# Performance work log

Hardware: AMD Instinct MI355X
Metric: run time of the kernel (lower is better)

The kernel has to match this reference:

```python
import jax, jax.numpy as jnp
import numpy as np

NEG_SLOPE = 0.2
EPS = 1e-5

N_NODES = 50000
N_GRAPHS = 500
NODES_PER_GRAPH = 100
N_EDGES = 500000
F_IN = 16
F_GRAPH = 4
HID = 64
N_CLASSES = 2


def setup_inputs() -> dict:
    key = jax.random.key(0)
    ks = jax.random.split(key, 32)
    x = jax.random.normal(ks[0], (N_NODES, F_IN), dtype=jnp.float32)
    # intra-graph random edges: dst lives in the same 100-node block as src
    src = jax.random.randint(ks[1], (N_EDGES,), 0, N_NODES)
    dst = (src // NODES_PER_GRAPH) * NODES_PER_GRAPH + jax.random.randint(ks[2], (N_EDGES,), 0, NODES_PER_GRAPH)
    edge_index = jnp.stack([src, dst]).astype(jnp.int64)
    graph_input = jax.random.normal(ks[3], (N_GRAPHS, F_GRAPH), dtype=jnp.float32)
    batch = (jnp.arange(N_NODES) // NODES_PER_GRAPH).astype(jnp.int64)

    def w(k, shape, scale=0.1):
        return (jax.random.normal(k, shape, dtype=jnp.float32) * scale)

    inp = dict(x=x, edge_index=edge_index, graph_input=graph_input, batch=batch)
    # GraphNorm params
    inp['gn_w'] = jnp.ones((F_IN,), jnp.float32)
    inp['gn_b'] = w(ks[4], (F_IN,))
    inp['gn_ms'] = jnp.ones((F_IN,), jnp.float32)
    inp['W1'] = w(ks[5], (F_IN, 4 * HID))
    inp['as1'] = w(ks[6], (4, HID)); inp['ad1'] = w(ks[7], (4, HID))
    inp['b1'] = w(ks[8], (4 * HID,))
    inp['W2'] = w(ks[9], (4 * HID, 4 * HID))
    inp['as2'] = w(ks[10], (4, HID)); inp['ad2'] = w(ks[11], (4, HID))
    inp['b2'] = w(ks[12], (4 * HID,))
    inp['W3'] = w(ks[13], (4 * HID, HID))
    inp['as3'] = w(ks[14], (1, HID)); inp['ad3'] = w(ks[15], (1, HID))
    inp['b3'] = w(ks[16], (HID,))
    # BatchNorm1d (eval mode) over [HID + F_GRAPH]
    D = HID + F_GRAPH
    inp['bn_g'] = 1.0 + w(ks[17], (D,))
    inp['bn_b'] = w(ks[18], (D,))
    inp['bn_m'] = jnp.zeros((D,), jnp.float32)
    inp['bn_v'] = jnp.ones((D,), jnp.float32)
    # Dense head
    inp['Wd1'] = w(ks[19], (D, HID)); inp['bd1'] = w(ks[20], (HID,))
    inp['Wd2'] = w(ks[21], (HID, HID)); inp['bd2'] = w(ks[22], (HID,))
    inp['Wo'] = w(ks[23], (HID, N_CLASSES)); inp['bo'] = w(ks[24], (N_CLASSES,))
    return inp


def _segment_softmax(e, seg, n):
    m = jax.ops.segment_max(e, seg, num_segments=n)
    ex = jnp.exp(e - m[seg])
    s = jax.ops.segment_sum(ex, seg, num_segments=n)
    return ex / s[seg]


def _gat_conv(x, src, dst, W, att_src, att_dst, b):
    N = x.shape[0]
    H, C = att_src.shape
    loop = jnp.arange(N)
    src = jnp.concatenate([src, loop])  # PyG GATConv adds self-loops
    dst = jnp.concatenate([dst, loop])
    h = (x @ W).reshape(N, H, C)
    a_src = (h * att_src).sum(-1)  # [N,H]
    a_dst = (h * att_dst).sum(-1)
    e = jax.nn.leaky_relu(a_src[src] + a_dst[dst], NEG_SLOPE)  # [E,H]
    alpha = _segment_softmax(e, dst, N)
    out = jax.ops.segment_sum(h[src] * alpha[:, :, None], dst, num_segments=N)
    return out.reshape(N, H * C) + b


def _graph_norm(x, batch, n_graphs, w, b, ms):
    cnt = jax.ops.segment_sum(jnp.ones((x.shape[0],), x.dtype), batch, num_segments=n_graphs)[:, None]
    mean = jax.ops.segment_sum(x, batch, num_segments=n_graphs) / cnt
    out = x - mean[batch] * ms
    var = jax.ops.segment_sum(out * out, batch, num_segments=n_graphs) / cnt
    return w * out / jnp.sqrt(var[batch] + EPS) + b


def _global_mean_pool(x, batch, n_graphs):
    cnt = jax.ops.segment_sum(jnp.ones((x.shape[0],), x.dtype), batch, num_segments=n_graphs)[:, None]
    return jax.ops.segment_sum(x, batch, num_segments=n_graphs) / cnt


def reference(x, edge_index, graph_input, batch,
              gn_w, gn_b, gn_ms,
              W1, as1, ad1, b1,
              W2, as2, ad2, b2,
              W3, as3, ad3, b3,
              bn_g, bn_b, bn_m, bn_v,
              Wd1, bd1, Wd2, bd2, Wo, bo):
    src, dst = edge_index[0], edge_index[1]
    G = graph_input.shape[0]
    h = _graph_norm(x, batch, G, gn_w, gn_b, gn_ms)
    # dropout is a no-op in eval
    h = jax.nn.elu(_gat_conv(h, src, dst, W1, as1, ad1, b1))
    h = jax.nn.elu(_gat_conv(h, src, dst, W2, as2, ad2, b2))
    h = _gat_conv(h, src, dst, W3, as3, ad3, b3)
    g = _global_mean_pool(h, batch, G)
    g = jnp.concatenate([g, graph_input], axis=1)
    g = (g - bn_m) / jnp.sqrt(bn_v + EPS) * bn_g + bn_b  # BatchNorm1d eval
    g = jax.nn.selu(g @ Wd1 + bd1)
    g = jax.nn.selu(g @ Wd2 + bd2)
    g = g @ Wo + bo
    return jax.nn.softmax(g, axis=1)
```

## Files before the change

### kernel.cpp

```cpp
#include <hip/hip_runtime.h>
#include <math.h>

#define N_NODES 50000
#define N_ROWS_PAD 50048
#define N_GRAPHS 500
#define NPG 100
#define N_EDGES 500000
#define F_IN 16
#define HID 64
#define EW_CAP 1408

#define SELU_SCALE 1.0507009873554804934193349852946f
#define SELU_ALPHA 1.6732632423543772848170429916717f

typedef __attribute__((ext_vector_type(8))) short short8;
typedef __attribute__((ext_vector_type(8))) unsigned short ushort8;
typedef __attribute__((ext_vector_type(4))) float floatx4;

__device__ __forceinline__ float lrelu(float x){ return x > 0.f ? x : 0.2f * x; }
__device__ __forceinline__ float eluf(float x){ return x > 0.f ? x : expf(x) - 1.f; }
__device__ __forceinline__ float seluf(float x){
    return x > 0.f ? SELU_SCALE * x : SELU_SCALE * (SELU_ALPHA * (expf(x) - 1.f));
}
__device__ __forceinline__ unsigned short f2bf(float x){
    unsigned u = __float_as_uint(x);
    return (unsigned short)((u + 0x7FFFu + ((u >> 16) & 1u)) >> 16);
}
__device__ __forceinline__ float bf2f(unsigned short u){
    return __uint_as_float((unsigned)u << 16);
}
__device__ __forceinline__ float bf2f_lo(unsigned u){
    return __uint_as_float(u << 16);
}
__device__ __forceinline__ float bf2f_hi(unsigned u){
    return __uint_as_float(u & 0xFFFF0000u);
}

__global__ void k_count(const int* __restrict__ dst, int* __restrict__ counts){
    int e = blockIdx.x * 256 + threadIdx.x;
    if (e < N_EDGES) atomicAdd(&counts[dst[e]], 1);
}

__global__ void __launch_bounds__(128)
k_local_scan(const int* __restrict__ counts, int* __restrict__ noff,
             int* __restrict__ cnt, int* __restrict__ write_ptr){
    __shared__ int s[128];
    int g = blockIdx.x, t = threadIdx.x;
    int v = (t < NPG) ? counts[g * NPG + t] : 0;
    s[t] = v; __syncthreads();
    for (int o = 1; o < 128; o <<= 1){
        int x = (t >= o) ? s[t - o] : 0;
        __syncthreads();
        s[t] += x;
        __syncthreads();
    }
    if (t < NPG){
        int excl = s[t] - v;
        noff[g * NPG + t] = excl;
        cnt[g * NPG + t] = v;
        write_ptr[g * NPG + t] = excl;
    }
}

__global__ void k_scatter(const int* __restrict__ src, const int* __restrict__ dst,
                          int* __restrict__ write_ptr, unsigned* __restrict__ csr){
    int e = blockIdx.x * 256 + threadIdx.x;
    if (e < N_EDGES){
        int d = dst[e];
        int g = d / NPG;
        int b = g * NPG;
        int pos = atomicAdd(&write_ptr[d], 1);
        csr[(size_t)g * EW_CAP + pos] = (unsigned)((src[e] - b) | ((d - b) << 8));
    }
}

__global__ void k_prep(const float* __restrict__ W1, const float* __restrict__ as1,
                       const float* __restrict__ ad1,
                       const float* __restrict__ W2, const float* __restrict__ as2,
                       const float* __restrict__ ad2,
                       const float* __restrict__ W3, const float* __restrict__ as3,
                       const float* __restrict__ ad3,
                       unsigned short* __restrict__ Wp2, unsigned short* __restrict__ Wp3,
                       float* __restrict__ M1f,
                       unsigned short* __restrict__ Mp2, unsigned short* __restrict__ Mp3){
    int id = blockIdx.x * 256 + threadIdx.x;
    if (id < 65536){
        int k = id >> 8, o = id & 255;
        int srccol = (o & 3) * 64 + (o >> 2);
        Wp2[(((k >> 3) * 256) + o) * 8 + (k & 7)] = f2bf(W2[k * 256 + srccol]);
    } else if (id < 81920){
        int i = id - 65536;
        int k = i >> 6, n = i & 63;
        Wp3[(((k >> 3) * 64) + n) * 8 + (k & 7)] = f2bf(W3[i]);
    } else if (id < 82048){
        int i = id - 81920;
        int k = i >> 3, j = i & 7;
        int h = j & 3;
        const float* a = (j < 4) ? as1 : ad1;
        float s = 0.f;
        for (int c = 0; c < 64; c++) s += W1[k * 256 + h * 64 + c] * a[h * 64 + c];
        M1f[k * 8 + j] = s;
    } else if (id < 86144){
        int i = id - 82048;
        int k = i >> 4, col = i & 15;
        float s = 0.f;
        if (col < 8){
            int h = col & 3;
            const float* a = (col < 4) ? as2 : ad2;
            for (int c = 0; c < 64; c++) s += W2[k * 256 + h * 64 + c] * a[h * 64 + c];
        }
        Mp2[((k >> 3) * 16 + col) * 8 + (k & 7)] = f2bf(s);
    } else if (id < 90240){
        int i = id - 86144;
        int k = i >> 4, col = i & 15;
        float s = 0.f;
        if (col < 2){
            const float* a = (col == 0) ? as3 : ad3;
            for (int c = 0; c < 64; c++) s += W3[k * 64 + c] * a[c];
        }
        Mp3[((k >> 3) * 16 + col) * 8 + (k & 7)] = f2bf(s);
    }
}

__global__ void __launch_bounds__(256)
k_gnorm_conv1(const float* __restrict__ x, const float* __restrict__ w,
              const float* __restrict__ b, const float* __restrict__ ms,
              const float* __restrict__ W1, const float* __restrict__ M1f,
              unsigned short* __restrict__ Ybf, float* __restrict__ lg1){
    __shared__ float sx[NPG * F_IN];
    __shared__ float Ws[16][256];
    __shared__ float red[16][16];
    __shared__ float meanS[16], varS[16];
    int g = blockIdx.x, t = threadIdx.x;
    int base = g * NPG;
    for (int idx = t; idx < NPG * F_IN; idx += 256) sx[idx] = x[base * F_IN + idx];
    for (int i = t; i < 1024; i += 256)
        *(float4*)&Ws[0][i * 4] = *(const float4*)&W1[i * 4];
    __syncthreads();
    int f = t & 15, grp = t >> 4;
    float p = 0.f;
    for (int i = grp; i < NPG; i += 16) p += sx[i * 16 + f];
    red[grp][f] = p; __syncthreads();
    if (t < 16){
        float s = 0.f;
        for (int i = 0; i < 16; i++) s += red[i][t];
        meanS[t] = s * (1.f / 100.f);
    }
    __syncthreads();
    float mm = meanS[f] * ms[f];
    p = 0.f;
    for (int i = grp; i < NPG; i += 16){ float v = sx[i * 16 + f] - mm; p += v * v; }
    red[grp][f] = p; __syncthreads();
    if (t < 16){
        float s = 0.f;
        for (int i = 0; i < 16; i++) s += red[i][t];
        varS[t] = s * (1.f / 100.f);
    }
    __syncthreads();
    for (int idx = t; idx < NPG * F_IN; idx += 256){
        int ff = idx & 15;
        sx[idx] = w[ff] * (sx[idx] - meanS[ff] * ms[ff]) * rsqrtf(varS[ff] + 1e-5f) + b[ff];
    }
    __syncthreads();
    int c4 = t & 15, rsub = t >> 4;
    for (int n = rsub; n < NPG; n += 16){
        float acc[16];
        #pragma unroll
        for (int j = 0; j < 16; j++) acc[j] = 0.f;
        #pragma unroll
        for (int k = 0; k < 16; k++){
            float a_ = sx[n * 16 + k];
            float4 b0 = *(const float4*)&Ws[k][c4 * 4];
            float4 b1 = *(const float4*)&Ws[k][64 + c4 * 4];
            float4 b2 = *(const float4*)&Ws[k][128 + c4 * 4];
            float4 b3 = *(const float4*)&Ws[k][192 + c4 * 4];
            float bv[16] = {b0.x, b0.y, b0.z, b0.w, b1.x, b1.y, b1.z, b1.w,
                            b2.x, b2.y, b2.z, b2.w, b3.x, b3.y, b3.z, b3.w};
            #pragma unroll
            for (int j = 0; j < 16; j++) acc[j] = fmaf(a_, bv[j], acc[j]);
        }
        ushort8 ua, ub;
        #pragma unroll
        for (int m = 0; m < 8; m++){
            ua[m] = f2bf(acc[(m & 3) * 4 + (m >> 2)]);
            ub[m] = f2bf(acc[(m & 3) * 4 + 2 + (m >> 2)]);
        }
        size_t ob = (size_t)(base + n) * 256 + c4 * 16;
        *(ushort8*)&Ybf[ob]     = ua;
        *(ushort8*)&Ybf[ob + 8] = ub;
    }
    for (int i = t; i < NPG * 8; i += 256){
        int n = i >> 3, j = i & 7;
        float s = 0.f;
        #pragma unroll
        for (int ff = 0; ff < 16; ff++) s += sx[n * 16 + ff] * M1f[ff * 8 + j];
        lg1[(size_t)(base + n) * 8 + j] = s;
    }
}

template<int COLB, int LG>
__global__ void __launch_bounds__(256)
k_gemm_mfma(const unsigned short* __restrict__ Xb,
            const unsigned short* __restrict__ Wp,
            const unsigned short* __restrict__ Mp,
            unsigned short* __restrict__ Ybf, float* __restrict__ lg,
            int N, int K, int OUT){
    int b = blockIdx.x;
    if (COLB == 4){
        int xcd = b & 7, idx = b >> 3;
        b = xcd * (int)(gridDim.x >> 3) + idx;
    }
    int cb = b & (COLB - 1);
    int rb = b / COLB;

    int t = threadIdx.x;
    int wave = t >> 6, lane = t & 63;
    int quad = lane >> 4, ln = lane & 15;
    int r0 = rb * 64 + wave * 16;
    int c0 = cb * 64;

    floatx4 acc[4];
    #pragma unroll
    for (int f = 0; f < 4; f++) acc[f] = (floatx4){0.f, 0.f, 0.f, 0.f};
    floatx4 accL = (floatx4){0.f, 0.f, 0.f, 0.f};

    const unsigned short* aptr = Xb + (size_t)(r0 + ln) * K + quad * 8;
    for (int kt = 0; kt < K; kt += 32){
        short8 a = *(const short8*)(aptr + kt);
        int kc = (kt >> 3) + quad;
        #pragma unroll
        for (int f = 0; f < 4; f++){
            short8 bfr = *(const short8*)(Wp + ((size_t)kc * OUT + c0 + f * 16 + ln) * 8);
            acc[f] = __builtin_amdgcn_mfma_f32_16x16x32_bf16(a, bfr, acc[f], 0, 0, 0);
        }
        if (LG > 0){
            if (cb == 0){
                short8 m = *(const short8*)(Mp + ((size_t)kc * 16 + ln) * 8);
                accL = __builtin_amdgcn_mfma_f32_16x16x32_bf16(a, m, accL, 0, 0, 0);
            }
        }
    }
    int rowb = r0 + quad * 4;
    #pragma unroll
    for (int f = 0; f < 4; f++){
        int col = c0 + f * 16 + ln;
        #pragma unroll
        for (int rg = 0; rg < 4; rg++){
            int row = rowb + rg;
            if (row < N) Ybf[(size_t)row * OUT + col] = f2bf(acc[f][rg]);
        }
    }
    if (LG > 0){
        if (cb == 0 && ln < LG){
            #pragma unroll
            for (int rg = 0; rg < 4; rg++){
                int row = rowb + rg;
                if (row < N) lg[(size_t)row * LG + ln] = accL[rg];
            }
        }
    }
}

__global__ void __launch_bounds__(512)
k_fused4(const unsigned short* __restrict__ hbf, const float* __restrict__ lg,
         const float* __restrict__ bias,
         const unsigned* __restrict__ csr, const int* __restrict__ noff,
         const int* __restrict__ cnt, unsigned short* __restrict__ out_bf){
    __shared__ __align__(16) unsigned int edl[EW_CAP][4];
    __shared__ __align__(16) float asrcl[NPG * 4], adstl[NPG * 4];
    __shared__ __align__(16) float wselfl[NPG * 4], rsuml[NPG * 4];
    __shared__ int offl[NPG], cntl[NPG];

    int g = blockIdx.x, t = threadIdx.x;
    int wave = t >> 6, lane = t & 63;
    int base = g * NPG;
    size_t ebeg = (size_t)g * EW_CAP;

    if (t < NPG){
        offl[t] = noff[base + t];
        cntl[t] = cnt[base + t];
        const float* lp = lg + (size_t)(base + t) * 8;
        *(float4*)&asrcl[t * 4] = *(const float4*)lp;
        *(float4*)&adstl[t * 4] = *(const float4*)(lp + 4);
    }
    __syncthreads();
    int eln = offl[NPG - 1] + cntl[NPG - 1];
    for (int i = t; i < eln; i += 512) edl[i][2] = csr[ebeg + i];
    __syncthreads();

    for (int i = t; i < eln; i += 512){
        unsigned sd = edl[i][2];
        int s = sd & 0xFF, d = sd >> 8;
        float4 av = *(const float4*)&asrcl[s * 4];
        float4 dv = *(const float4*)&adstl[d * 4];
        unsigned w0 = f2bf(expf(lrelu(av.x + dv.x)));
        unsigned w1 = f2bf(expf(lrelu(av.y + dv.y)));
        unsigned w2 = f2bf(expf(lrelu(av.z + dv.z)));
        unsigned w3 = f2bf(expf(lrelu(av.w + dv.w)));
        edl[i][0] = w0 | (w1 << 16);
        edl[i][1] = w2 | (w3 << 16);
    }
    __syncthreads();

    if (t < NPG){
        int d = t;
        float4 av = *(const float4*)&asrcl[d * 4];
        float4 dv = *(const float4*)&adstl[d * 4];
        float ws0 = expf(lrelu(av.x + dv.x));
        float ws1 = expf(lrelu(av.y + dv.y));
        float ws2 = expf(lrelu(av.z + dv.z));
        float ws3 = expf(lrelu(av.w + dv.w));
        float s0 = ws0, s1 = ws1, s2 = ws2, s3 = ws3;
        int ebg = offl[d], n = cntl[d];
        for (int j = 0; j < n; j++){
            uint2 v = *(const uint2*)&edl[ebg + j][0];
            s0 += bf2f_lo(v.x); s1 += bf2f_hi(v.x);
            s2 += bf2f_lo(v.y); s3 += bf2f_hi(v.y);
        }
        *(float4*)&wselfl[d * 4] = make_float4(ws0, ws1, ws2, ws3);
        *(float4*)&rsuml[d * 4]  = make_float4(1.f / s0, 1.f / s1, 1.f / s2, 1.f / s3);
    }
    __syncthreads();

    float b0 = bias[lane], b1 = bias[64 + lane], b2 = bias[128 + lane], b3 = bias[192 + lane];
    for (int d = wave; d < NPG; d += 8){
        float4 ws = *(const float4*)&wselfl[d * 4];
        float4 rs = *(const float4*)&rsuml[d * 4];
        ushort4 hv = *(const ushort4*)&hbf[(size_t)(base + d) * 256 + lane * 4];
        float a0 = ws.x * bf2f(hv.x);
        float a1 = ws.y * bf2f(hv.y);
        float a2 = ws.z * bf2f(hv.z);
        float a3 = ws.w * bf2f(hv.w);
        int ebg = offl[d], n = cntl[d];
        int j = 0;
        #pragma unroll 1
        for (; j + 4 <= n; j += 4){
            #pragma unroll
            for (int k = 0; k < 4; k++){
                uint4 v = *(const uint4*)&edl[ebg + j + k][0];
                int s = (int)(v.z & 0xFFu);
                ushort4 x = *(const ushort4*)&hbf[(size_t)(base + s) * 256 + lane * 4];
                a0 = fmaf(bf2f_lo(v.x), bf2f(x.x), a0);
                a1 = fmaf(bf2f_hi(v.x), bf2f(x.y), a1);
                a2 = fmaf(bf2f_lo(v.y), bf2f(x.z), a2);
                a3 = fmaf(bf2f_hi(v.y), bf2f(x.w), a3);
            }
        }
        for (; j < n; j++){
            uint4 v = *(const uint4*)&edl[ebg + j][0];
            int s = (int)(v.z & 0xFFu);
            ushort4 x = *(const ushort4*)&hbf[(size_t)(base + s) * 256 + lane * 4];
            a0 = fmaf(bf2f_lo(v.x), bf2f(x.x), a0);
            a1 = fmaf(bf2f_hi(v.x), bf2f(x.y), a1);
            a2 = fmaf(bf2f_lo(v.y), bf2f(x.z), a2);
            a3 = fmaf(bf2f_hi(v.y), bf2f(x.w), a3);
        }
        size_t ob = (size_t)(base + d) * 256 + lane;
        out_bf[ob]       = f2bf(eluf(a0 * rs.x + b0));
        out_bf[ob + 64]  = f2bf(eluf(a1 * rs.y + b1));
        out_bf[ob + 128] = f2bf(eluf(a2 * rs.z + b2));
        out_bf[ob + 192] = f2bf(eluf(a3 * rs.w + b3));
    }
}

__global__ void __launch_bounds__(512)
k_fused1(const unsigned short* __restrict__ hbf, const float* __restrict__ lg3,
         const float* __restrict__ bias,
         const unsigned* __restrict__ csr, const int* __restrict__ noff,
         const int* __restrict__ cnt, float* __restrict__ out){
    __shared__ __align__(16) unsigned int edl[EW_CAP][2];
    __shared__ float asrcl[NPG], adstl[NPG];
    __shared__ float wselfl[NPG], rsuml[NPG];
    __shared__ int offl[NPG], cntl[NPG];

    int g = blockIdx.x, t = threadIdx.x;
    int wave = t >> 6, lane = t & 63;
    int base = g * NPG;
    size_t ebeg = (size_t)g * EW_CAP;

    if (t < NPG){
        offl[t] = noff[base + t];
        cntl[t] = cnt[base + t];
        asrcl[t] = lg3[(size_t)(base + t) * 2];
        adstl[t] = lg3[(size_t)(base + t) * 2 + 1];
    }
    __syncthreads();
    int eln = offl[NPG - 1] + cntl[NPG - 1];
    for (int i = t; i < eln; i += 512) edl[i][1] = csr[ebeg + i];
    __syncthreads();

    for (int i = t; i < eln; i += 512){
        unsigned sd = edl[i][1];
        int s = sd & 0xFF, d = sd >> 8;
        edl[i][0] = (unsigned)f2bf(expf(lrelu(asrcl[s] + adstl[d])));
    }
    __syncthreads();

    if (t < NPG){
        float wsf = expf(lrelu(asrcl[t] + adstl[t]));
        float sum = wsf;
        int ebg = offl[t], n = cntl[t];
        for (int j = 0; j < n; j++) sum += bf2f((unsigned short)edl[ebg + j][0]);
        wselfl[t] = wsf;
        rsuml[t] = 1.f / sum;
    }
    __syncthreads();

    float bl = bias[lane];
    for (int d = wave; d < NPG; d += 8){
        float acc = wselfl[d] * bf2f(hbf[(size_t)(base + d) * 64 + lane]);
        int ebg = offl[d], n = cntl[d];
        for (int j = 0; j < n; j++){
            uint2 v = *(const uint2*)&edl[ebg + j][0];
            acc = fmaf(bf2f_lo(v.x),
                       bf2f(hbf[(size_t)(base + (int)(v.y & 0xFFu)) * 64 + lane]), acc);
        }
        out[(size_t)(base + d) * 64 + lane] = acc * rsuml[d] + bl;
    }
}

__global__ void k_head(const float* __restrict__ x3, const float* __restrict__ gin,
                       const float* __restrict__ bn_g, const float* __restrict__ bn_b,
                       const float* __restrict__ bn_m, const float* __restrict__ bn_v,
                       const float* __restrict__ Wd1, const float* __restrict__ bd1,
                       const float* __restrict__ Wd2, const float* __restrict__ bd2,
                       const float* __restrict__ Wo, const float* __restrict__ bo,
                       float* __restrict__ out){
    __shared__ float red[256];
    __shared__ float gv[68];
    __shared__ float g2[64];
    __shared__ float g3[64];
    int g = blockIdx.x, t = threadIdx.x;
    int c = t & 63, grp = t >> 6;
    float p = 0.f;
    for (int i = grp; i < NPG; i += 4) p += x3[(g * NPG + i) * 64 + c];
    red[t] = p; __syncthreads();
    if (t < 64){
        float s = red[t] + red[t + 64] + red[t + 128] + red[t + 192];
        float mean = s * (1.f / 100.f);
        gv[t] = (mean - bn_m[t]) * rsqrtf(bn_v[t] + 1e-5f) * bn_g[t] + bn_b[t];
    } else if (t < 68){
        int j = t - 64;
        float v = gin[g * 4 + j];
        gv[t] = (v - bn_m[t]) * rsqrtf(bn_v[t] + 1e-5f) * bn_g[t] + bn_b[t];
    }
    __syncthreads();
    if (t < 64){
        float s = bd1[t];
        for (int i = 0; i < 68; i++) s += gv[i] * Wd1[i * 64 + t];
        g2[t] = seluf(s);
    }
    __syncthreads();
    if (t < 64){
        float s = bd2[t];
        for (int i = 0; i < 64; i++) s += g2[i] * Wd2[i * 64 + t];
        g3[t] = seluf(s);
    }
    __syncthreads();
    if (t == 0){
        float l0 = bo[0], l1 = bo[1];
        for (int i = 0; i < 64; i++){ l0 += g3[i] * Wo[i * 2]; l1 += g3[i] * Wo[i * 2 + 1]; }
        float mx = fmaxf(l0, l1);
        float e0 = expf(l0 - mx), e1 = expf(l1 - mx);
        float inv = 1.f / (e0 + e1);
        out[g * 2] = e0 * inv;
        out[g * 2 + 1] = e1 * inv;
    }
}

extern "C" void kernel_launch(void* const* d_in, const int* in_sizes, int n_in,
                              void* d_out, int out_size, void* d_ws, size_t ws_size,
                              hipStream_t stream){
    const float* x   = (const float*)d_in[0];
    const int*   ei  = (const int*)d_in[1];
    const float* gin = (const float*)d_in[2];
    const float* gn_w = (const float*)d_in[4];
    const float* gn_b = (const float*)d_in[5];
    const float* gn_ms = (const float*)d_in[6];
    const float* W1 = (const float*)d_in[7];
    const float* as1 = (const float*)d_in[8];
    const float* ad1 = (const float*)d_in[9];
    const float* b1 = (const float*)d_in[10];
    const float* W2 = (const float*)d_in[11];
    const float* as2 = (const float*)d_in[12];
    const float* ad2 = (const float*)d_in[13];
    const float* b2 = (const float*)d_in[14];
    const float* W3 = (const float*)d_in[15];
    const float* as3 = (const float*)d_in[16];
    const float* ad3 = (const float*)d_in[17];
    const float* b3 = (const float*)d_in[18];
    const float* bn_g = (const float*)d_in[19];
    const float* bn_b = (const float*)d_in[20];
    const float* bn_m = (const float*)d_in[21];
    const float* bn_v = (const float*)d_in[22];
    const float* Wd1 = (const float*)d_in[23];
    const float* bd1 = (const float*)d_in[24];
    const float* Wd2 = (const float*)d_in[25];
    const float* bd2 = (const float*)d_in[26];
    const float* Wo = (const float*)d_in[27];
    const float* bo = (const float*)d_in[28];
    float* out = (float*)d_out;

    const int* src = ei;
    const int* dst = ei + N_EDGES;

    char* ws = (char*)d_ws;
    size_t off = 0;
    auto alloc = [&](size_t bytes) -> void* {
        void* p = ws + off;
        off = (off + bytes + 255) & ~(size_t)255;
        return p;
    };
    int* counts     = (int*)alloc((size_t)N_NODES * 4);
    int* write_ptr  = (int*)alloc((size_t)N_NODES * 4);
    unsigned* csr   = (unsigned*)alloc((size_t)N_GRAPHS * EW_CAP * 4);
    int* noff       = (int*)alloc((size_t)N_NODES * 4);
    int* cnt        = (int*)alloc((size_t)N_NODES * 4);
    unsigned short* wp2 = (unsigned short*)alloc((size_t)256 * 256 * 2);
    unsigned short* wp3 = (unsigned short*)alloc((size_t)256 * 64 * 2);
    float* M1f      = (float*)alloc((size_t)16 * 8 * 4);
    unsigned short* Mp2 = (unsigned short*)alloc((size_t)32 * 16 * 8 * 2);
    unsigned short* Mp3 = (unsigned short*)alloc((size_t)32 * 16 * 8 * 2);
    float* lg1      = (float*)alloc((size_t)N_NODES * 8 * 4);
    float* lg2      = (float*)alloc((size_t)N_ROWS_PAD * 8 * 4);
    float* lg3      = (float*)alloc((size_t)N_ROWS_PAD * 2 * 4);
    unsigned short* xbh = (unsigned short*)alloc((size_t)N_NODES * 256 * 2);
    unsigned short* xb  = (unsigned short*)alloc((size_t)N_ROWS_PAD * 256 * 2);
    unsigned short* x3b = (unsigned short*)alloc((size_t)N_NODES * HID * 2);
    float* bufD     = (float*)alloc((size_t)N_NODES * HID * 4);

    hipMemsetAsync(counts, 0, (size_t)N_NODES * 4, stream);
    k_count<<<(N_EDGES + 255) / 256, 256, 0, stream>>>(dst, counts);
    k_prep<<<(90240 + 255) / 256, 256, 0, stream>>>(W1, as1, ad1, W2, as2, ad2,
                                                    W3, as3, ad3, wp2, wp3, M1f, Mp2, Mp3);
    k_local_scan<<<N_GRAPHS, 128, 0, stream>>>(counts, noff, cnt, write_ptr);
    k_scatter<<<(N_EDGES + 255) / 256, 256, 0, stream>>>(src, dst, write_ptr, csr);

    k_gnorm_conv1<<<N_GRAPHS, 256, 0, stream>>>(x, gn_w, gn_b, gn_ms, W1, M1f, xbh, lg1);
    k_fused4<<<N_GRAPHS, 512, 0, stream>>>(xbh, lg1, b1, csr, noff, cnt, xb);

    k_gemm_mfma<4, 8><<<(N_ROWS_PAD / 64) * 4, 256, 0, stream>>>(xb, wp2, Mp2, xbh, lg2,
                                                                 N_NODES, 256, 256);
    k_fused4<<<N_GRAPHS, 512, 0, stream>>>(xbh, lg2, b2, csr, noff, cnt, xb);

    k_gemm_mfma<1, 2><<<N_ROWS_PAD / 64, 256, 0, stream>>>(xb, wp3, Mp3, x3b, lg3,
                                                           N_NODES, 256, 64);
    k_fused1<<<N_GRAPHS, 512, 0, stream>>>(x3b, lg3, b3, csr, noff, cnt, bufD);

    k_head<<<N_GRAPHS, 256, 0, stream>>>(bufD, gin, bn_g, bn_b, bn_m, bn_v,
                                         Wd1, bd1, Wd2, bd2, Wo, bo, out);
}
```

Measured before the change: 340.9 us.

## Fuse layer-3 GEMM, GAT aggregation, pooling and dense head into one kernel

Replaces the final MFMA GEMM, the single-head GAT aggregation kernel and the head kernel with one per-graph kernel. Seven waves compute the 100x64 projection and attention logits with MFMA straight into shared memory, while the eighth wave loads CSR data. Aggregation then reads neighbours from LDS and mean-pools in registers, so the x3b, lg3 and bufD round trips and two launches go away. The cost is that rows 100-111 of the MFMA tile read into the next graph's rows (harmless, since they are masked), plus higher LDS use per block, which may lower occupancy.

```diff
diff --git a/kernel.cpp b/kernel.cpp
--- a/kernel.cpp
+++ b/kernel.cpp
@@ -364,30 +364,77 @@
 }
 
 __global__ void __launch_bounds__(512)
-k_fused1(const unsigned short* __restrict__ hbf, const float* __restrict__ lg3,
-         const float* __restrict__ bias,
-         const unsigned* __restrict__ csr, const int* __restrict__ noff,
-         const int* __restrict__ cnt, float* __restrict__ out){
+k_tail(const unsigned short* __restrict__ xb, const unsigned short* __restrict__ Wp3,
+       const unsigned short* __restrict__ Mp3, const float* __restrict__ bias,
+       const unsigned* __restrict__ csr, const int* __restrict__ noff,
+       const int* __restrict__ cnt, const float* __restrict__ gin,
+       const float* __restrict__ bn_g, const float* __restrict__ bn_b,
+       const float* __restrict__ bn_m, const float* __restrict__ bn_v,
+       const float* __restrict__ Wd1, const float* __restrict__ bd1,
+       const float* __restrict__ Wd2, const float* __restrict__ bd2,
+       const float* __restrict__ Wo, const float* __restrict__ bo,
+       float* __restrict__ out){
+    __shared__ __align__(16) unsigned short h3[NPG * 64];
     __shared__ __align__(16) unsigned int edl[EW_CAP][2];
     __shared__ float asrcl[NPG], adstl[NPG];
     __shared__ float wselfl[NPG], rsuml[NPG];
     __shared__ int offl[NPG], cntl[NPG];
+    __shared__ float red[8][64];
+    __shared__ float gv[68], g2[64], g3[64];
 
     int g = blockIdx.x, t = threadIdx.x;
     int wave = t >> 6, lane = t & 63;
     int base = g * NPG;
     size_t ebeg = (size_t)g * EW_CAP;
 
-    if (t < NPG){
-        offl[t] = noff[base + t];
-        cntl[t] = cnt[base + t];
-        asrcl[t] = lg3[(size_t)(base + t) * 2];
-        adstl[t] = lg3[(size_t)(base + t) * 2 + 1];
+    if (wave < 7){
+        int quad = lane >> 4, ln = lane & 15;
+        floatx4 acc[4];
+        #pragma unroll
+        for (int f = 0; f < 4; f++) acc[f] = (floatx4){0.f, 0.f, 0.f, 0.f};
+        floatx4 accL = (floatx4){0.f, 0.f, 0.f, 0.f};
+        const unsigned short* aptr = xb + (size_t)(base + wave * 16 + ln) * 256 + quad * 8;
+        for (int kt = 0; kt < 256; kt += 32){
+            short8 a = *(const short8*)(aptr + kt);
+            int kc = (kt >> 3) + quad;
+            #pragma unroll
+            for (int f = 0; f < 4; f++){
+                short8 bfr = *(const short8*)(Wp3 + ((size_t)kc * 64 + f * 16 + ln) * 8);
+                acc[f] = __builtin_amdgcn_mfma_f32_16x16x32_bf16(a, bfr, acc[f], 0, 0, 0);
+            }
+            short8 m = *(const short8*)(Mp3 + ((size_t)kc * 16 + ln) * 8);
+            accL = __builtin_amdgcn_mfma_f32_16x16x32_bf16(a, m, accL, 0, 0, 0);
+        }
+        int rowb = wave * 16 + quad * 4;
+        #pragma unroll
+        for (int f = 0; f < 4; f++){
+            int col = f * 16 + ln;
+            #pragma unroll
+            for (int rg = 0; rg < 4; rg++){
+                int row = rowb + rg;
+                if (row < NPG) h3[row * 64 + col] = f2bf(acc[f][rg]);
+            }
+        }
+        if (ln < 2){
+            #pragma unroll
+            for (int rg = 0; rg < 4; rg++){
+                int row = rowb + rg;
+                if (row < NPG){
+                    if (ln == 0) asrcl[row] = accL[rg];
+                    else         adstl[row] = accL[rg];
+                }
+            }
+        }
+    } else {
+        for (int i = lane; i < NPG; i += 64){
+            offl[i] = noff[base + i];
+            cntl[i] = cnt[base + i];
+        }
+        int el = noff[base + NPG - 1] + cnt[base + NPG - 1];
+        for (int i = lane; i < el; i += 64) edl[i][1] = csr[ebeg + i];
     }
     __syncthreads();
     int eln = offl[NPG - 1] + cntl[NPG - 1];
-    for (int i = t; i < eln; i += 512) edl[i][1] = csr[ebeg + i];
-    __syncthreads();
 
     for (int i = t; i < eln; i += 512){
         unsigned sd = edl[i][1];
@@ -407,36 +454,23 @@
     __syncthreads();
 
     float bl = bias[lane];
+    float pool = 0.f;
     for (int d = wave; d < NPG; d += 8){
-        float acc = wselfl[d] * bf2f(hbf[(size_t)(base + d) * 64 + lane]);
+        float acc = wselfl[d] * bf2f(h3[d * 64 + lane]);
         int ebg = offl[d], n = cntl[d];
         for (int j = 0; j < n; j++){
             uint2 v = *(const uint2*)&edl[ebg + j][0];
-            acc = fmaf(bf2f_lo(v.x),
-                       bf2f(hbf[(size_t)(base + (int)(v.y & 0xFFu)) * 64 + lane]), acc);
-        }
-        out[(size_t)(base + d) * 64 + lane] = acc * rsuml[d] + bl;
-    }
-}
-
-__global__ void k_head(const float* __restrict__ x3, const float* __restrict__ gin,
-                       const float* __restrict__ bn_g, const float* __restrict__ bn_b,
-                       const float* __restrict__ bn_m, const float* __restrict__ bn_v,
-                       const float* __restrict__ Wd1, const float* __restrict__ bd1,
-                       const float* __restrict__ Wd2, const float* __restrict__ bd2,
-                       const float* __restrict__ Wo, const float* __restrict__ bo,
-                       float* __restrict__ out){
-    __shared__ float red[256];
-    __shared__ float gv[68];
-    __shared__ float g2[64];
-    __shared__ float g3[64];
-    int g = blockIdx.x, t = threadIdx.x;
-    int c = t & 63, grp = t >> 6;
-    float p = 0.f;
-    for (int i = grp; i < NPG; i += 4) p += x3[(g * NPG + i) * 64 + c];
-    red[t] = p; __syncthreads();
+            acc = fmaf(bf2f_lo(v.x), bf2f(h3[(int)(v.y & 0xFFu) * 64 + lane]), acc);
+        }
+        pool += acc * rsuml[d] + bl;
+    }
+    red[wave][lane] = pool;
+    __syncthreads();
+
     if (t < 64){
-        float s = red[t] + red[t + 64] + red[t + 128] + red[t + 192];
+        float s = 0.f;
+        #pragma unroll
+        for (int i = 0; i < 8; i++) s += red[i][t];
         float mean = s * (1.f / 100.f);
         gv[t] = (mean - bn_m[t]) * rsqrtf(bn_v[t] + 1e-5f) * bn_g[t] + bn_b[t];
     } else if (t < 68){
@@ -523,11 +557,8 @@
     unsigned short* Mp3 = (unsigned short*)alloc((size_t)32 * 16 * 8 * 2);
     float* lg1      = (float*)alloc((size_t)N_NODES * 8 * 4);
     float* lg2      = (float*)alloc((size_t)N_ROWS_PAD * 8 * 4);
-    float* lg3      = (float*)alloc((size_t)N_ROWS_PAD * 2 * 4);
     unsigned short* xbh = (unsigned short*)alloc((size_t)N_NODES * 256 * 2);
     unsigned short* xb  = (unsigned short*)alloc((size_t)N_ROWS_PAD * 256 * 2);
-    unsigned short* x3b = (unsigned short*)alloc((size_t)N_NODES * HID * 2);
-    float* bufD     = (float*)alloc((size_t)N_NODES * HID * 4);
 
     hipMemsetAsync(counts, 0, (size_t)N_NODES * 4, stream);
     k_count<<<(N_EDGES + 255) / 256, 256, 0, stream>>>(dst, counts);
@@ -543,10 +574,7 @@
                                                                  N_NODES, 256, 256);
     k_fused4<<<N_GRAPHS, 512, 0, stream>>>(xbh, lg2, b2, csr, noff, cnt, xb);
 
-    k_gemm_mfma<1, 2><<<N_ROWS_PAD / 64, 256, 0, stream>>>(xb, wp3, Mp3, x3b, lg3,
-                                                           N_NODES, 256, 64);
-    k_fused1<<<N_GRAPHS, 512, 0, stream>>>(x3b, lg3, b3, csr, noff, cnt, bufD);
-
-    k_head<<<N_GRAPHS, 256, 0, stream>>>(bufD, gin, bn_g, bn_b, bn_m, bn_v,
+    k_tail<<<N_GRAPHS, 512, 0, stream>>>(xb, wp3, Mp3, b3, csr, noff, cnt, gin,
+                                         bn_g, bn_b, bn_m, bn_v,
                                          Wd1, bd1, Wd2, bd2, Wo, bo, out);
 }
```

Result: faster. 315.8 us (-7.4%).
